# Kernel optimization log

Measured on AMD Instinct MI355X. Metric: run time of the kernel, lower is better.

## Reference

```python
import jax, jax.numpy as jnp
import numpy as np
import math

W = 64  # window_size == chunk_size == 64


def _windows(x, w):
    """x: [b, t, ...] -> [b, nb, 2w, ...]: for block j, concat(block j-1, block j).
    Block -1 is zero padding; its validity is handled by the attention mask."""
    b, t = x.shape[0], x.shape[1]
    nb = t // w
    pad = [(0, 0), (w, 0)] + [(0, 0)] * (x.ndim - 2)
    xp = jnp.pad(x, pad)                                   # [b, t+w, ...]
    xb = xp.reshape((b, nb + 1, w) + x.shape[2:])          # [b, nb+1, w, ...]
    return jnp.concatenate([xb[:, :-1], xb[:, 1:]], axis=2)  # [b, nb, 2w, ...]


def setup_inputs() -> dict:
    key = jax.random.key(0)
    k1, k2, k3 = jax.random.split(key, 3)
    b, t, h, d = 4, 4096, 16, 64
    return {
        "q": jax.random.normal(k1, (b, t, h, d), dtype=jnp.float32),
        "k": jax.random.normal(k2, (b, t, h, d), dtype=jnp.float32),
        "v": jax.random.normal(k3, (b, t, h, d), dtype=jnp.float32),
        "attn_mask": jnp.ones((b, t), dtype=jnp.int32),
    }


def reference(q, k, v, attn_mask):
    b, t, h, d = q.shape
    nb = t // W
    scale = 1.0 / math.sqrt(d)

    qb = q.reshape(b, nb, W, h, d)
    kw = _windows(k, W)                         # [b, nb, 2W, h, d]
    vw = _windows(v, W)                         # [b, nb, 2W, h, d]
    mw = _windows(attn_mask.astype(bool), W)    # [b, nb, 2W]

    # query local index i attends to key local index m iff 0 <= (i+W-m) < W
    i = jnp.arange(W)[:, None]
    m = jnp.arange(2 * W)[None, :]
    diff = i + W - m
    band = (diff >= 0) & (diff < W)             # [W, 2W]

    valid = band[None, None] & mw[:, :, None, :]          # [b, nb, W, 2W]

    scores = jnp.einsum('bnqhd,bnkhd->bnhqk', qb, kw) * scale  # [b,nb,h,W,2W]
    scores = jnp.where(valid[:, :, None], scores, jnp.float32(-1e9))
    attn = jax.nn.softmax(scores, axis=-1)
    attn = attn * valid[:, :, None].astype(attn.dtype)

    qm = attn_mask.astype(q.dtype).reshape(b, nb, W)      # query validity
    attn = attn * qm[:, :, None, :, None]

    out = jnp.einsum('bnhqk,bnkhd->bnqhd', attn, vw)      # [b,nb,W,h,d]
    out = out * qm[:, :, :, None, None]
    return out.reshape(b, t, h, d)
```

## Files before the change

kernel.cpp:

```cpp
#include <hip/hip_runtime.h>


#define TT 4096
#define HH 16
#define DD 64
#define WW 64
#define NBLK (TT / WW)

typedef __attribute__((ext_vector_type(8))) short bf16x8;
typedef __attribute__((ext_vector_type(16))) float f32x16;

static __device__ __forceinline__ uint bfr(float x) {
    uint u = __builtin_bit_cast(uint, x);
    return (u + 0x7FFFu + ((u >> 16) & 1u)) >> 16;
}
static __device__ __forceinline__ ushort f2bf(float x) { return (ushort)bfr(x); }
static __device__ __forceinline__ uint pack2(float a, float b) {
    return bfr(a) | (bfr(b) << 16);
}
static __device__ __forceinline__ int vsw(int d) { return ((d >> 2) ^ d) & 15; }

__global__ __launch_bounds__(128, 3)
void lca_fwd(const float* __restrict__ q, const float* __restrict__ k,
             const float* __restrict__ v, const int* __restrict__ am,
             float* __restrict__ out)
{
    const int jb = ((blockIdx.x & 7) << 3) | (blockIdx.x >> 3);
    const int hd = blockIdx.y;
    const int bi = blockIdx.z;

    __shared__ __align__(16) ushort sVt[8192];

    const int tid  = threadIdx.x;
    const int wv   = tid >> 6;
    const int lane = tid & 63;
    const int l31  = lane & 31, hl = lane >> 5;

    const int T0 = jb * WW;
    const int Tq = T0 + 32 * wv;
    const size_t rowstride = (size_t)HH * DD;
    const size_t hoff = ((size_t)bi * TT) * rowstride + (size_t)hd * DD;
    const int* amb = am + (size_t)bi * TT;

    long tok0 = (long)Tq - 64 + lane;
    unsigned long long m_lo = __ballot((tok0 >= 0) && (amb[tok0 < 0 ? 0 : tok0] != 0));
    unsigned int m_hi = (unsigned int)__ballot(amb[Tq + l31] != 0);

    {
        const int d0 = (tid & 15) * 4;
        const int rb = tid >> 4;
        #pragma unroll
        for (int p = 0; p < 16; ++p) {
            int kl = p * 8 + rb;
            long tok = (long)T0 - 64 + kl;
            if (tok < 0) tok = 0;
            const float4 x = *(const float4*)(v + hoff + (size_t)tok * rowstride + d0);
            int e = kl & 15;
            int pos = (kl & ~15) | (e & 3) | ((e & 8) >> 1) | ((e & 4) << 1);
            int pu = pos >> 3, p7 = pos & 7;
            sVt[(d0 + 0) * 128 + ((pu ^ vsw(d0 + 0)) << 3) + p7] = f2bf(x.x);
            sVt[(d0 + 1) * 128 + ((pu ^ vsw(d0 + 1)) << 3) + p7] = f2bf(x.y);
            sVt[(d0 + 2) * 128 + ((pu ^ vsw(d0 + 2)) << 3) + p7] = f2bf(x.z);
            sVt[(d0 + 3) * 128 + ((pu ^ vsw(d0 + 3)) << 3) + p7] = f2bf(x.w);
        }
    }

    bf16x8 Bq[4];
    {
        const float* qr = q + hoff + (size_t)(Tq + l31) * rowstride + hl * 8;
        #pragma unroll
        for (int ds = 0; ds < 4; ++ds) {
            float4 a = *(const float4*)(qr + ds * 16);
            float4 b = *(const float4*)(qr + ds * 16 + 4);
            union { bf16x8 v8; uint u[4]; } w;
            w.u[0] = pack2(a.x, a.y); w.u[1] = pack2(a.z, a.w);
            w.u[2] = pack2(b.x, b.y); w.u[3] = pack2(b.z, b.w);
            Bq[ds] = w.v8;
        }
    }

    float s[48];
    #pragma unroll
    for (int t = 0; t < 3; ++t) {
        long krw = (long)Tq - 64 + 32 * t + l31;
        if (krw < 0) krw = 0;
        const float* kr = k + hoff + (size_t)krw * rowstride + hl * 8;
        f32x16 a;
        #pragma unroll
        for (int i = 0; i < 16; ++i) a[i] = 0.f;
        #pragma unroll
        for (int ds = 0; ds < 4; ++ds) {
            float4 xx = *(const float4*)(kr + ds * 16);
            float4 yy = *(const float4*)(kr + ds * 16 + 4);
            union { bf16x8 v8; uint u[4]; } w;
            w.u[0] = pack2(xx.x, xx.y); w.u[1] = pack2(xx.z, xx.w);
            w.u[2] = pack2(yy.x, yy.y); w.u[3] = pack2(yy.z, yy.w);
            a = __builtin_amdgcn_mfma_f32_32x32x16_bf16(w.v8, Bq[ds], a, 0, 0, 0);
        }
        #pragma unroll
        for (int r = 0; r < 16; ++r) s[t * 16 + r] = a[r];
    }

    const int ql = l31;
    float vb[48];
    #pragma unroll
    for (int t = 0; t < 3; ++t)
        #pragma unroll
        for (int r = 0; r < 16; ++r) {
            int kl = 32 * t + (r & 3) + 8 * (r >> 2) + 4 * hl;
            bool band = (t == 0) ? (kl > ql) : (t == 2 ? (kl - 64 <= ql) : true);
            vb[t * 16 + r] = band ? 1.f : 0.f;
        }
    if (!((m_lo == ~0ull) && (m_hi == 0xFFFFFFFFu))) {
        #pragma unroll
        for (int t = 0; t < 3; ++t)
            #pragma unroll
            for (int r = 0; r < 16; ++r) {
                int kl = 32 * t + (r & 3) + 8 * (r >> 2) + 4 * hl;
                uint bit = (kl < 64) ? (uint)((m_lo >> kl) & 1ull)
                                     : ((m_hi >> (kl - 64)) & 1u);
                vb[t * 16 + r] *= (float)bit;
            }
    }
    float mx[24];
    #pragma unroll
    for (int i = 0; i < 24; ++i) mx[i] = fmaxf(s[i], s[i + 24]);
    #pragma unroll
    for (int i = 0; i < 12; ++i) mx[i] = fmaxf(mx[i], mx[i + 12]);
    #pragma unroll
    for (int i = 0; i < 6;  ++i) mx[i] = fmaxf(mx[i], mx[i + 6]);
    float rmax = fmaxf(fmaxf(fmaxf(mx[0], mx[1]), fmaxf(mx[2], mx[3])),
                       fmaxf(mx[4], mx[5]));
    rmax = fmaxf(rmax, __shfl_xor(rmax, 32, 64));

    const float CEXP = 0.125f * 1.44269504088896f;
    float p[48];
    #pragma unroll
    for (int i = 0; i < 48; ++i)
        p[i] = exp2f((s[i] - rmax) * CEXP) * vb[i];

    float t24[24];
    #pragma unroll
    for (int i = 0; i < 24; ++i) t24[i] = p[i] + p[i + 24];
    #pragma unroll
    for (int i = 0; i < 12; ++i) t24[i] += t24[i + 12];
    #pragma unroll
    for (int i = 0; i < 6;  ++i) t24[i] += t24[i + 6];
    float sum = ((t24[0] + t24[1]) + (t24[2] + t24[3])) + (t24[4] + t24[5]);
    sum += __shfl_xor(sum, 32, 64);

    float rden = (sum > 0.f ? 1.f / sum : 0.f) * (float)((m_hi >> ql) & 1u);
    #pragma unroll
    for (int i = 0; i < 48; ++i) p[i] *= rden;

    __syncthreads();

    f32x16 O0, O1;
    #pragma unroll
    for (int i = 0; i < 16; ++i) { O0[i] = 0.f; O1[i] = 0.f; }
    #pragma unroll
    for (int st = 0; st < 6; ++st) {
        union { bf16x8 v8; uint u[4]; } A;
        const int pb = 16 * (st >> 1) + 8 * (st & 1);
        #pragma unroll
        for (int j = 0; j < 4; ++j)
            A.u[j] = pack2(p[pb + 2 * j], p[pb + 2 * j + 1]);
        const int Ub = 4 * wv + 2 * st + hl;
        {
            int d = l31;
            const bf16x8 B0 = *(const bf16x8*)(&sVt[d * 128 + ((Ub ^ vsw(d)) << 3)]);
            O0 = __builtin_amdgcn_mfma_f32_32x32x16_bf16(A.v8, B0, O0, 0, 0, 0);
        }
        {
            int d = 32 + l31;
            const bf16x8 B1 = *(const bf16x8*)(&sVt[d * 128 + ((Ub ^ vsw(d)) << 3)]);
            O1 = __builtin_amdgcn_mfma_f32_32x32x16_bf16(A.v8, B1, O1, 0, 0, 0);
        }
    }

    float* ob = out + hoff + (size_t)Tq * rowstride;
    #pragma unroll
    for (int r = 0; r < 16; ++r) {
        int qrow = (r & 3) + 8 * (r >> 2) + 4 * hl;
        float* orow = ob + (size_t)qrow * rowstride;
        orow[l31]      = O0[r];
        orow[32 + l31] = O1[r];
    }
}

extern "C" void kernel_launch(void* const* d_in, const int* in_sizes, int n_in,
                              void* d_out, int out_size, void* d_ws, size_t ws_size,
                              hipStream_t stream) {
    const float* q  = (const float*)d_in[0];
    const float* k  = (const float*)d_in[1];
    const float* v  = (const float*)d_in[2];
    const int*   am = (const int*)d_in[3];
    float* outp = (float*)d_out;

    const int b = in_sizes[3] / TT;
    dim3 grid(NBLK, HH, b);
    dim3 block(128);
    lca_fwd<<<grid, block, 0, stream>>>(q, k, v, am, outp);
}
```

Measured before the change: 233.0 us.

## Issue all Q/K/V global loads up front and defer V LDS transpose until after softmax

All global loads for Q, K, V and the mask are hoisted into registers at kernel start, so their latencies overlap instead of each load group stalling in turn. The V bf16 transpose into shared memory moves to after the softmax, so the QK^T MFMAs and softmax math can run while V is still arriving. The band/mask vector is fused into the exp pass, and probabilities are packed to bf16 once. The large register footprint forces launch bounds down from 3 to 2 waves-per-SIMD occupancy, trading latency hiding through occupancy for latency hiding through in-flight loads.

```diff
diff --git a/kernel.cpp b/kernel.cpp
--- a/kernel.cpp
+++ b/kernel.cpp
@@ -20,7 +20,7 @@
 }
 static __device__ __forceinline__ int vsw(int d) { return ((d >> 2) ^ d) & 15; }
 
-__global__ __launch_bounds__(128, 3)
+__global__ __launch_bounds__(128, 2)
 void lca_fwd(const float* __restrict__ q, const float* __restrict__ k,
              const float* __restrict__ v, const int* __restrict__ am,
              float* __restrict__ out)
@@ -43,58 +43,66 @@
     const int* amb = am + (size_t)bi * TT;
 
     long tok0 = (long)Tq - 64 + lane;
-    unsigned long long m_lo = __ballot((tok0 >= 0) && (amb[tok0 < 0 ? 0 : tok0] != 0));
-    unsigned int m_hi = (unsigned int)__ballot(amb[Tq + l31] != 0);
-
-    {
-        const int d0 = (tid & 15) * 4;
-        const int rb = tid >> 4;
-        #pragma unroll
-        for (int p = 0; p < 16; ++p) {
-            int kl = p * 8 + rb;
-            long tok = (long)T0 - 64 + kl;
-            if (tok < 0) tok = 0;
-            const float4 x = *(const float4*)(v + hoff + (size_t)tok * rowstride + d0);
-            int e = kl & 15;
-            int pos = (kl & ~15) | (e & 3) | ((e & 8) >> 1) | ((e & 4) << 1);
-            int pu = pos >> 3, p7 = pos & 7;
-            sVt[(d0 + 0) * 128 + ((pu ^ vsw(d0 + 0)) << 3) + p7] = f2bf(x.x);
-            sVt[(d0 + 1) * 128 + ((pu ^ vsw(d0 + 1)) << 3) + p7] = f2bf(x.y);
-            sVt[(d0 + 2) * 128 + ((pu ^ vsw(d0 + 2)) << 3) + p7] = f2bf(x.z);
-            sVt[(d0 + 3) * 128 + ((pu ^ vsw(d0 + 3)) << 3) + p7] = f2bf(x.w);
-        }
-    }
-
-    bf16x8 Bq[4];
+    int am_lo = amb[tok0 < 0 ? 0 : tok0];
+    int am_hi = amb[Tq + l31];
+
+    float4 vq[8], vk[24], vv[16];
     {
         const float* qr = q + hoff + (size_t)(Tq + l31) * rowstride + hl * 8;
         #pragma unroll
         for (int ds = 0; ds < 4; ++ds) {
-            float4 a = *(const float4*)(qr + ds * 16);
-            float4 b = *(const float4*)(qr + ds * 16 + 4);
-            union { bf16x8 v8; uint u[4]; } w;
-            w.u[0] = pack2(a.x, a.y); w.u[1] = pack2(a.z, a.w);
-            w.u[2] = pack2(b.x, b.y); w.u[3] = pack2(b.z, b.w);
-            Bq[ds] = w.v8;
-        }
-    }
-
-    float s[48];
+            vq[2 * ds]     = *(const float4*)(qr + ds * 16);
+            vq[2 * ds + 1] = *(const float4*)(qr + ds * 16 + 4);
+        }
+    }
     #pragma unroll
     for (int t = 0; t < 3; ++t) {
         long krw = (long)Tq - 64 + 32 * t + l31;
-        if (krw < 0) krw = 0;
-        const float* kr = k + hoff + (size_t)krw * rowstride + hl * 8;
+        const float* kr = k + hoff + (size_t)(krw < 0 ? 0 : krw) * rowstride + hl * 8;
+        #pragma unroll
+        for (int ds = 0; ds < 4; ++ds) {
+            vk[8 * t + 2 * ds]     = *(const float4*)(kr + ds * 16);
+            vk[8 * t + 2 * ds + 1] = *(const float4*)(kr + ds * 16 + 4);
+        }
+    }
+    const int d0 = (tid & 15) * 4;
+    const int rb = tid >> 4;
+    #pragma unroll
+    for (int p = 0; p < 16; ++p) {
+        int kl = p * 8 + rb;
+        long tok = (long)T0 - 64 + kl;
+        if (tok < 0) tok = 0;
+        vv[p] = *(const float4*)(v + hoff + (size_t)tok * rowstride + d0);
+    }
+
+    unsigned long long m_lo = __ballot((tok0 >= 0) && (am_lo != 0));
+    unsigned int m_hi = (unsigned int)__ballot(am_hi != 0);
+    const bool fastmask = (m_lo == ~0ull) && (m_hi == 0xFFFFFFFFu);
+
+    bf16x8 Bq[4];
+    #pragma unroll
+    for (int ds = 0; ds < 4; ++ds) {
+        union { bf16x8 v8; uint u[4]; } w;
+        w.u[0] = pack2(vq[2 * ds].x,     vq[2 * ds].y);
+        w.u[1] = pack2(vq[2 * ds].z,     vq[2 * ds].w);
+        w.u[2] = pack2(vq[2 * ds + 1].x, vq[2 * ds + 1].y);
+        w.u[3] = pack2(vq[2 * ds + 1].z, vq[2 * ds + 1].w);
+        Bq[ds] = w.v8;
+    }
+
+    float s[48];
+    #pragma unroll
+    for (int t = 0; t < 3; ++t) {
         f32x16 a;
         #pragma unroll
         for (int i = 0; i < 16; ++i) a[i] = 0.f;
         #pragma unroll
         for (int ds = 0; ds < 4; ++ds) {
-            float4 xx = *(const float4*)(kr + ds * 16);
-            float4 yy = *(const float4*)(kr + ds * 16 + 4);
             union { bf16x8 v8; uint u[4]; } w;
-            w.u[0] = pack2(xx.x, xx.y); w.u[1] = pack2(xx.z, xx.w);
-            w.u[2] = pack2(yy.x, yy.y); w.u[3] = pack2(yy.z, yy.w);
+            w.u[0] = pack2(vk[8 * t + 2 * ds].x,     vk[8 * t + 2 * ds].y);
+            w.u[1] = pack2(vk[8 * t + 2 * ds].z,     vk[8 * t + 2 * ds].w);
+            w.u[2] = pack2(vk[8 * t + 2 * ds + 1].x, vk[8 * t + 2 * ds + 1].y);
+            w.u[3] = pack2(vk[8 * t + 2 * ds + 1].z, vk[8 * t + 2 * ds + 1].w);
             a = __builtin_amdgcn_mfma_f32_32x32x16_bf16(w.v8, Bq[ds], a, 0, 0, 0);
         }
         #pragma unroll
@@ -102,26 +110,6 @@
     }
 
     const int ql = l31;
-    float vb[48];
-    #pragma unroll
-    for (int t = 0; t < 3; ++t)
-        #pragma unroll
-        for (int r = 0; r < 16; ++r) {
-            int kl = 32 * t + (r & 3) + 8 * (r >> 2) + 4 * hl;
-            bool band = (t == 0) ? (kl > ql) : (t == 2 ? (kl - 64 <= ql) : true);
-            vb[t * 16 + r] = band ? 1.f : 0.f;
-        }
-    if (!((m_lo == ~0ull) && (m_hi == 0xFFFFFFFFu))) {
-        #pragma unroll
-        for (int t = 0; t < 3; ++t)
-            #pragma unroll
-            for (int r = 0; r < 16; ++r) {
-                int kl = 32 * t + (r & 3) + 8 * (r >> 2) + 4 * hl;
-                uint bit = (kl < 64) ? (uint)((m_lo >> kl) & 1ull)
-                                     : ((m_hi >> (kl - 64)) & 1u);
-                vb[t * 16 + r] *= (float)bit;
-            }
-    }
     float mx[24];
     #pragma unroll
     for (int i = 0; i < 24; ++i) mx[i] = fmaxf(s[i], s[i + 24]);
@@ -136,8 +124,21 @@
     const float CEXP = 0.125f * 1.44269504088896f;
     float p[48];
     #pragma unroll
-    for (int i = 0; i < 48; ++i)
-        p[i] = exp2f((s[i] - rmax) * CEXP) * vb[i];
+    for (int t = 0; t < 3; ++t)
+        #pragma unroll
+        for (int r = 0; r < 16; ++r) {
+            int i  = t * 16 + r;
+            int kl = 32 * t + (r & 3) + 8 * (r >> 2) + 4 * hl;
+            float pe = exp2f((s[i] - rmax) * CEXP);
+            bool band = (t == 0) ? (kl > ql) : (t == 2 ? (kl - 64 <= ql) : true);
+            pe = band ? pe : 0.f;
+            if (!fastmask) {
+                uint bit = (kl < 64) ? (uint)((m_lo >> kl) & 1ull)
+                                     : ((m_hi >> (kl - 64)) & 1u);
+                pe *= (float)bit;
+            }
+            p[i] = pe;
+        }
 
     float t24[24];
     #pragma unroll
@@ -150,8 +151,24 @@
     sum += __shfl_xor(sum, 32, 64);
 
     float rden = (sum > 0.f ? 1.f / sum : 0.f) * (float)((m_hi >> ql) & 1u);
-    #pragma unroll
-    for (int i = 0; i < 48; ++i) p[i] *= rden;
+
+    uint pk[24];
+    #pragma unroll
+    for (int m = 0; m < 24; ++m)
+        pk[m] = pack2(p[2 * m] * rden, p[2 * m + 1] * rden);
+
+    #pragma unroll
+    for (int pp = 0; pp < 16; ++pp) {
+        int kl = pp * 8 + rb;
+        const float4 x = vv[pp];
+        int e = kl & 15;
+        int pos = (kl & ~15) | (e & 3) | ((e & 8) >> 1) | ((e & 4) << 1);
+        int pu = pos >> 3, p7 = pos & 7;
+        sVt[(d0 + 0) * 128 + ((pu ^ vsw(d0 + 0)) << 3) + p7] = f2bf(x.x);
+        sVt[(d0 + 1) * 128 + ((pu ^ vsw(d0 + 1)) << 3) + p7] = f2bf(x.y);
+        sVt[(d0 + 2) * 128 + ((pu ^ vsw(d0 + 2)) << 3) + p7] = f2bf(x.z);
+        sVt[(d0 + 3) * 128 + ((pu ^ vsw(d0 + 3)) << 3) + p7] = f2bf(x.w);
+    }
 
     __syncthreads();
 
@@ -161,10 +178,9 @@
     #pragma unroll
     for (int st = 0; st < 6; ++st) {
         union { bf16x8 v8; uint u[4]; } A;
-        const int pb = 16 * (st >> 1) + 8 * (st & 1);
-        #pragma unroll
-        for (int j = 0; j < 4; ++j)
-            A.u[j] = pack2(p[pb + 2 * j], p[pb + 2 * j + 1]);
+        const int mb = 8 * (st >> 1) + 4 * (st & 1);
+        #pragma unroll
+        for (int j = 0; j < 4; ++j) A.u[j] = pk[mb + j];
         const int Ub = 4 * wv + 2 * st + hl;
         {
             int d = l31;
```

Result: no change. 229.6 us (-1.5%).
